# Performance work log

Hardware: AMD Instinct MI355X
Metric: run time of the kernel (lower is better)

The kernel has to match this reference:

```python
import jax, jax.numpy as jnp
import numpy as np

N, D, S, H, NH, HD, K = 1, 17, 128, 2048, 16, 128, 16
Dp = D - 1          # chunks with history (q[:, 1:])
Sk = 128            # kv chunk length
EPS = 1e-6


def setup_inputs() -> dict:
    key = jax.random.key(0)
    k0, k1, k2, k3, k4, k5 = jax.random.split(key, 6)
    return {
        "hidden_states": jax.random.normal(k0, (N, D, S, H), jnp.float32),
        "chunk_k": jax.random.normal(k1, (N * Dp * K, Sk, NH, HD), jnp.float32),
        "chunk_v": jax.random.normal(k2, (N * Dp * K, Sk, NH, HD), jnp.float32),
        "weights": jax.random.uniform(k3, (N, Dp, K), jnp.float32),
        "rms_weight": jnp.ones((H,), jnp.float32),
        "Wq": jax.random.normal(k4, (H, H), jnp.float32) * 0.02,
        "Wo": jax.random.normal(k5, (H, H), jnp.float32) * 0.02,
    }


def reference(hidden_states, chunk_k, chunk_v, weights, rms_weight, Wq, Wo):
    # RMSNorm (pre_norm)
    var = jnp.mean(hidden_states * hidden_states, axis=-1, keepdims=True)
    xn = hidden_states * jax.lax.rsqrt(var + EPS) * rms_weight
    # q projection: Linear stores (out, in) -> x @ W.T
    q = jnp.einsum('ndsh,eh->ndse', xn, Wq).reshape(N, D, S, NH, HD)
    # chunk_size (= D) > 1: drop the first chunk (no history)
    qd = q[:, 1:]                                      # (N, Dp, S, NH, HD)
    k = chunk_k.reshape(N, Dp, K, Sk, NH, HD)
    v = chunk_v.reshape(N, Dp, K, Sk, NH, HD)
    scale = 1.0 / np.sqrt(HD)
    # non-causal flash attention per (N, Dp, K) chunk
    scores = jnp.einsum('ndshe,ndkthe->ndkhst', qd, k) * scale
    p = jax.nn.softmax(scores, axis=-1)
    vals = jnp.einsum('ndkhst,ndkthe->ndkhse', p, v)   # (N, Dp, K, NH, S, HD)
    # weighted reduction over K history chunks
    wv = jnp.einsum('ndkhse,ndk->ndhse', vals, weights)
    o = wv.transpose(0, 1, 3, 2, 4).reshape(N, Dp * S, H)  # N (D S) (h d)
    o = jnp.einsum('nsh,eh->nse', o, Wo)
    # pad: first chunk (S = enc_chunk_size + 1 positions) gets zeros
    ret = jnp.zeros((N, D * S, H), o.dtype)
    ret = ret.at[:, -Dp * S:, :].set(o)
    return ret
```

## Files before the change

### kernel.cpp

```cpp
#include <hip/hip_runtime.h>
#include <hip/hip_bf16.h>
#include <math.h>


typedef __attribute__((ext_vector_type(8))) short bf16x8;
typedef __attribute__((ext_vector_type(4))) short bf16x4;
typedef __attribute__((ext_vector_type(4))) float f32x4;

__device__ __forceinline__ unsigned short f2bf(float f) {
    union { float f; unsigned u; } c; c.f = f;
    unsigned u = c.u + 0x7FFF + ((c.u >> 16) & 1);
    return (unsigned short)(u >> 16);
}

__global__ __launch_bounds__(256) void rms_kernel(const float* __restrict__ hs,
                                                  const float* __restrict__ rw,
                                                  unsigned short* __restrict__ xn) {
    int row = blockIdx.x;
    const float* x = hs + (size_t)(row + 128) * 2048;
    int tid = threadIdx.x;
    float4 a = ((const float4*)x)[tid * 2];
    float4 b = ((const float4*)x)[tid * 2 + 1];
    float ss = a.x*a.x + a.y*a.y + a.z*a.z + a.w*a.w
             + b.x*b.x + b.y*b.y + b.z*b.z + b.w*b.w;
#pragma unroll
    for (int m = 1; m < 64; m <<= 1) ss += __shfl_xor(ss, m);
    __shared__ float part[4];
    if ((tid & 63) == 0) part[tid >> 6] = ss;
    __syncthreads();
    float tot = part[0] + part[1] + part[2] + part[3];
    float rstd = rsqrtf(tot * (1.0f / 2048.0f) + 1e-6f);
    float4 wa = ((const float4*)rw)[tid * 2];
    float4 wb = ((const float4*)rw)[tid * 2 + 1];
    bf16x8 o;
    o[0] = (short)f2bf(a.x * rstd * wa.x);
    o[1] = (short)f2bf(a.y * rstd * wa.y);
    o[2] = (short)f2bf(a.z * rstd * wa.z);
    o[3] = (short)f2bf(a.w * rstd * wa.w);
    o[4] = (short)f2bf(b.x * rstd * wb.x);
    o[5] = (short)f2bf(b.y * rstd * wb.y);
    o[6] = (short)f2bf(b.z * rstd * wb.z);
    o[7] = (short)f2bf(b.w * rstd * wb.w);
    *reinterpret_cast<bf16x8*>(&xn[(size_t)row * 2048 + tid * 8]) = o;
}

__global__ __launch_bounds__(256) void cast_kernel(const float* __restrict__ in,
                                                   unsigned short* __restrict__ out) {
    size_t i = ((size_t)blockIdx.x * 256 + threadIdx.x) * 8;
    float4 a = *reinterpret_cast<const float4*>(in + i);
    float4 b = *reinterpret_cast<const float4*>(in + i + 4);
    bf16x8 o;
    o[0] = (short)f2bf(a.x); o[1] = (short)f2bf(a.y);
    o[2] = (short)f2bf(a.z); o[3] = (short)f2bf(a.w);
    o[4] = (short)f2bf(b.x); o[5] = (short)f2bf(b.y);
    o[6] = (short)f2bf(b.z); o[7] = (short)f2bf(b.w);
    *reinterpret_cast<bf16x8*>(out + i) = o;
}

template<int OUT_BF16>
__global__ __launch_bounds__(256) void gemm_bt(const unsigned short* __restrict__ A,
                                               const unsigned short* __restrict__ B,
                                               unsigned short* __restrict__ Cb,
                                               float* __restrict__ Cf) {
    __shared__ short As[128 * 72];
    __shared__ short Bs[128 * 72];
    int bm = (blockIdx.x >> 4) * 128;
    int bn = (blockIdx.x & 15) * 128;
    int tid = threadIdx.x;
    int lane = tid & 63, wid = tid >> 6;
    int wm = (wid >> 1) * 64, wn = (wid & 1) * 64;
    int r16 = lane & 15, g = lane >> 4;
    f32x4 acc[4][4] = {};

    for (int kt = 0; kt < 2048; kt += 64) {
#pragma unroll
        for (int p = 0; p < 4; ++p) {
            int idx = tid + p * 256;
            int r = idx >> 3, c = (idx & 7) * 8;
            *reinterpret_cast<bf16x8*>(&As[r * 72 + c]) =
                *reinterpret_cast<const bf16x8*>(&A[(size_t)(bm + r) * 2048 + kt + c]);
            *reinterpret_cast<bf16x8*>(&Bs[r * 72 + c]) =
                *reinterpret_cast<const bf16x8*>(&B[(size_t)(bn + r) * 2048 + kt + c]);
        }
        __syncthreads();
#pragma unroll
        for (int ks = 0; ks < 2; ++ks) {
            bf16x8 af[4], bfr[4];
#pragma unroll
            for (int i = 0; i < 4; ++i) {
                af[i]  = *reinterpret_cast<const bf16x8*>(&As[(wm + i * 16 + r16) * 72 + ks * 32 + g * 8]);
                bfr[i] = *reinterpret_cast<const bf16x8*>(&Bs[(wn + i * 16 + r16) * 72 + ks * 32 + g * 8]);
            }
#pragma unroll
            for (int i = 0; i < 4; ++i)
#pragma unroll
                for (int j = 0; j < 4; ++j)
                    acc[i][j] = __builtin_amdgcn_mfma_f32_16x16x32_bf16(af[i], bfr[j], acc[i][j], 0, 0, 0);
        }
        __syncthreads();
    }
#pragma unroll
    for (int i = 0; i < 4; ++i) {
        int row0 = bm + wm + i * 16 + g * 4;
#pragma unroll
        for (int j = 0; j < 4; ++j) {
            int col = bn + wn + j * 16 + r16;
#pragma unroll
            for (int rr = 0; rr < 4; ++rr) {
                float v = acc[i][j][rr];
                if (OUT_BF16) Cb[(size_t)(row0 + rr) * 2048 + col] = f2bf(v);
                else          Cf[(size_t)(row0 + rr) * 2048 + col] = v;
            }
        }
    }
}

__global__ __launch_bounds__(512) void attn_kernel(const unsigned short* __restrict__ q2d,
                                                   const float* __restrict__ ck,
                                                   const float* __restrict__ cv,
                                                   const float* __restrict__ wts,
                                                   unsigned short* __restrict__ o2d) {
    int dp = blockIdx.x >> 4;
    int h  = blockIdx.x & 15;
    int tid = threadIdx.x;
    int lane = tid & 63, w = tid >> 6;
    int r16 = lane & 15, g = lane >> 4;

    __shared__ short kbuf[128 * 136];
    __shared__ short vtbuf[128 * 136];
    __shared__ short pbuf[128 * 136];

    bf16x8 qf[4];
    {
        const unsigned short* qrow = q2d + (size_t)(dp * 128 + w * 16 + r16) * 2048 + h * 128 + g * 8;
#pragma unroll
        for (int ks = 0; ks < 4; ++ks)
            qf[ks] = *reinterpret_cast<const bf16x8*>(qrow + ks * 32);
    }
    f32x4 oacc[8] = {};
    const float sc = 0.088388347648318447f * 1.44269504088896f;

    for (int k = 0; k < 16; ++k) {
        size_t cbase = (size_t)(dp * 16 + k) * 128 * 2048 + h * 128;
#pragma unroll
        for (int p = 0; p < 8; ++p) {
            int t = p * 16 + (tid >> 5);
            int hd0 = (tid & 31) * 4;
            float4 v = *reinterpret_cast<const float4*>(&ck[cbase + (size_t)t * 2048 + hd0]);
            bf16x4 s4;
            s4[0] = (short)f2bf(v.x); s4[1] = (short)f2bf(v.y);
            s4[2] = (short)f2bf(v.z); s4[3] = (short)f2bf(v.w);
            *reinterpret_cast<bf16x4*>(&kbuf[t * 136 + hd0]) = s4;
        }
        {
            int hd = tid & 127;
            int tg = tid >> 7;
#pragma unroll
            for (int p = 0; p < 4; ++p) {
                int t0 = p * 32 + tg * 8;
                bf16x8 s8;
#pragma unroll
                for (int j = 0; j < 8; ++j)
                    s8[j] = (short)f2bf(cv[cbase + (size_t)(t0 + j) * 2048 + hd]);
                *reinterpret_cast<bf16x8*>(&vtbuf[hd * 136 + t0]) = s8;
            }
        }
        __syncthreads();

        f32x4 sacc[8] = {};
#pragma unroll
        for (int ks = 0; ks < 4; ++ks) {
#pragma unroll
            for (int nb = 0; nb < 8; ++nb) {
                bf16x8 kf = *reinterpret_cast<const bf16x8*>(&kbuf[(nb * 16 + r16) * 136 + ks * 32 + g * 8]);
                sacc[nb] = __builtin_amdgcn_mfma_f32_16x16x32_bf16(qf[ks], kf, sacc[nb], 0, 0, 0);
            }
        }

        float wdk = wts[dp * 16 + k];
        float fac[4];
#pragma unroll
        for (int r = 0; r < 4; ++r) {
            float m = sacc[0][r];
#pragma unroll
            for (int nb = 1; nb < 8; ++nb) m = fmaxf(m, sacc[nb][r]);
            m = fmaxf(m, __shfl_xor(m, 1));
            m = fmaxf(m, __shfl_xor(m, 2));
            m = fmaxf(m, __shfl_xor(m, 4));
            m = fmaxf(m, __shfl_xor(m, 8));
            float s = 0.f;
#pragma unroll
            for (int nb = 0; nb < 8; ++nb) {
                float p = exp2f((sacc[nb][r] - m) * sc);
                sacc[nb][r] = p;
                s += p;
            }
            s += __shfl_xor(s, 1);
            s += __shfl_xor(s, 2);
            s += __shfl_xor(s, 4);
            s += __shfl_xor(s, 8);
            fac[r] = wdk / s;
        }
#pragma unroll
        for (int r = 0; r < 4; ++r)
#pragma unroll
            for (int nb = 0; nb < 8; ++nb)
                pbuf[(w * 16 + g * 4 + r) * 136 + nb * 16 + r16] = (short)f2bf(sacc[nb][r] * fac[r]);

#pragma unroll
        for (int ks = 0; ks < 4; ++ks) {
            bf16x8 pf = *reinterpret_cast<const bf16x8*>(&pbuf[(w * 16 + r16) * 136 + ks * 32 + g * 8]);
#pragma unroll
            for (int nb = 0; nb < 8; ++nb) {
                bf16x8 vf = *reinterpret_cast<const bf16x8*>(&vtbuf[(nb * 16 + r16) * 136 + ks * 32 + g * 8]);
                oacc[nb] = __builtin_amdgcn_mfma_f32_16x16x32_bf16(pf, vf, oacc[nb], 0, 0, 0);
            }
        }
        __syncthreads();
    }

#pragma unroll
    for (int nb = 0; nb < 8; ++nb) {
#pragma unroll
        for (int rr = 0; rr < 4; ++rr) {
            int row = dp * 128 + w * 16 + g * 4 + rr;
            int col = h * 128 + nb * 16 + r16;
            o2d[(size_t)row * 2048 + col] = f2bf(oacc[nb][rr]);
        }
    }
}

extern "C" void kernel_launch(void* const* d_in, const int* in_sizes, int n_in,
                              void* d_out, int out_size, void* d_ws, size_t ws_size,
                              hipStream_t stream) {
    const float* hs  = (const float*)d_in[0];
    const float* ck  = (const float*)d_in[1];
    const float* cv  = (const float*)d_in[2];
    const float* wts = (const float*)d_in[3];
    const float* rw  = (const float*)d_in[4];
    const float* Wq  = (const float*)d_in[5];
    const float* Wo  = (const float*)d_in[6];
    float* out = (float*)d_out;

    char* ws = (char*)d_ws;
    unsigned short* xn  = (unsigned short*)(ws);
    unsigned short* wqb = (unsigned short*)(ws + (8u  << 20));
    unsigned short* qb  = (unsigned short*)(ws + (16u << 20));
    unsigned short* o2d = xn;
    unsigned short* wob = wqb;

    hipMemsetAsync(out, 0, (size_t)128 * 2048 * 4, stream);

    cast_kernel<<<2048, 256, 0, stream>>>(Wq, wqb);
    rms_kernel<<<2048, 256, 0, stream>>>(hs, rw, xn);
    gemm_bt<1><<<256, 256, 0, stream>>>(xn, wqb, qb, nullptr);
    attn_kernel<<<256, 512, 0, stream>>>(qb, ck, cv, wts, o2d);
    cast_kernel<<<2048, 256, 0, stream>>>(Wo, wob);
    gemm_bt<0><<<256, 256, 0, stream>>>(o2d, wob, nullptr, out + (size_t)128 * 2048);
}
```

Before: 659.2 us.

## Split-K GEMMs with atomic accumulation, LDS direct loads, and K/V register prefetch

Both projection GEMMs become a split-K kernel that launches 512 blocks instead of 256, each covering half of K and accumulating into zero-initialised fp32 output with atomicAdd. Tiles are loaded with global_load_lds straight into unpadded LDS. The q projection now lands in fp32 and is cast to bf16 inside attention. The attention kernel prefetches the next chunk's K/V into registers while computing the current one. The aim is better CU occupancy and overlap of loads with compute, at the cost of atomics, extra memsets, unpadded LDS bank conflicts and higher register pressure.

```diff
diff --git a/kernel.cpp b/kernel.cpp
--- a/kernel.cpp
+++ b/kernel.cpp
@@ -11,6 +11,11 @@
     union { float f; unsigned u; } c; c.f = f;
     unsigned u = c.u + 0x7FFF + ((c.u >> 16) & 1);
     return (unsigned short)(u >> 16);
+}
+
+__device__ __forceinline__ void gload16(const void* g, void* l) {
+    __builtin_amdgcn_global_load_lds((const __attribute__((address_space(1))) void*)g,
+                                     (__attribute__((address_space(3))) void*)l, 16, 0, 0);
 }
 
 __global__ __launch_bounds__(256) void rms_kernel(const float* __restrict__ hs,
@@ -57,30 +62,29 @@
     *reinterpret_cast<bf16x8*>(out + i) = o;
 }
 
-template<int OUT_BF16>
-__global__ __launch_bounds__(256) void gemm_bt(const unsigned short* __restrict__ A,
-                                               const unsigned short* __restrict__ B,
-                                               unsigned short* __restrict__ Cb,
-                                               float* __restrict__ Cf) {
-    __shared__ short As[128 * 72];
-    __shared__ short Bs[128 * 72];
-    int bm = (blockIdx.x >> 4) * 128;
-    int bn = (blockIdx.x & 15) * 128;
+__global__ __launch_bounds__(256, 2) void gemm_ks(const unsigned short* __restrict__ A,
+                                                  const unsigned short* __restrict__ B,
+                                                  float* __restrict__ C) {
+    __shared__ short As[128 * 64];
+    __shared__ short Bs[128 * 64];
+    int bid = blockIdx.x;
+    int ksl = bid & 1;
+    int bn = ((bid >> 1) & 15) * 128;
+    int bm = (bid >> 5) * 128;
     int tid = threadIdx.x;
     int lane = tid & 63, wid = tid >> 6;
     int wm = (wid >> 1) * 64, wn = (wid & 1) * 64;
     int r16 = lane & 15, g = lane >> 4;
     f32x4 acc[4][4] = {};
-
-    for (int kt = 0; kt < 2048; kt += 64) {
+    int k0 = ksl * 1024;
+
+    for (int kt = k0; kt < k0 + 1024; kt += 64) {
 #pragma unroll
         for (int p = 0; p < 4; ++p) {
-            int idx = tid + p * 256;
+            int idx = p * 256 + tid;
             int r = idx >> 3, c = (idx & 7) * 8;
-            *reinterpret_cast<bf16x8*>(&As[r * 72 + c]) =
-                *reinterpret_cast<const bf16x8*>(&A[(size_t)(bm + r) * 2048 + kt + c]);
-            *reinterpret_cast<bf16x8*>(&Bs[r * 72 + c]) =
-                *reinterpret_cast<const bf16x8*>(&B[(size_t)(bn + r) * 2048 + kt + c]);
+            gload16(&A[(size_t)(bm + r) * 2048 + kt + c], (void*)&As[idx * 8]);
+            gload16(&B[(size_t)(bn + r) * 2048 + kt + c], (void*)&Bs[idx * 8]);
         }
         __syncthreads();
 #pragma unroll
@@ -88,8 +92,8 @@
             bf16x8 af[4], bfr[4];
 #pragma unroll
             for (int i = 0; i < 4; ++i) {
-                af[i]  = *reinterpret_cast<const bf16x8*>(&As[(wm + i * 16 + r16) * 72 + ks * 32 + g * 8]);
-                bfr[i] = *reinterpret_cast<const bf16x8*>(&Bs[(wn + i * 16 + r16) * 72 + ks * 32 + g * 8]);
+                af[i]  = *reinterpret_cast<const bf16x8*>(&As[(wm + i * 16 + r16) * 64 + ks * 32 + g * 8]);
+                bfr[i] = *reinterpret_cast<const bf16x8*>(&Bs[(wn + i * 16 + r16) * 64 + ks * 32 + g * 8]);
             }
 #pragma unroll
             for (int i = 0; i < 4; ++i)
@@ -106,20 +110,17 @@
         for (int j = 0; j < 4; ++j) {
             int col = bn + wn + j * 16 + r16;
 #pragma unroll
-            for (int rr = 0; rr < 4; ++rr) {
-                float v = acc[i][j][rr];
-                if (OUT_BF16) Cb[(size_t)(row0 + rr) * 2048 + col] = f2bf(v);
-                else          Cf[(size_t)(row0 + rr) * 2048 + col] = v;
-            }
-        }
-    }
-}
-
-__global__ __launch_bounds__(512) void attn_kernel(const unsigned short* __restrict__ q2d,
-                                                   const float* __restrict__ ck,
-                                                   const float* __restrict__ cv,
-                                                   const float* __restrict__ wts,
-                                                   unsigned short* __restrict__ o2d) {
+            for (int rr = 0; rr < 4; ++rr)
+                atomicAdd(&C[(size_t)(row0 + rr) * 2048 + col], acc[i][j][rr]);
+        }
+    }
+}
+
+__global__ __launch_bounds__(512, 2) void attn_kernel(const float* __restrict__ qf,
+                                                      const float* __restrict__ ck,
+                                                      const float* __restrict__ cv,
+                                                      const float* __restrict__ wts,
+                                                      unsigned short* __restrict__ o2d) {
     int dp = blockIdx.x >> 4;
     int h  = blockIdx.x & 15;
     int tid = threadIdx.x;
@@ -130,42 +131,74 @@
     __shared__ short vtbuf[128 * 136];
     __shared__ short pbuf[128 * 136];
 
-    bf16x8 qf[4];
+    bf16x8 qfr[4];
     {
-        const unsigned short* qrow = q2d + (size_t)(dp * 128 + w * 16 + r16) * 2048 + h * 128 + g * 8;
-#pragma unroll
-        for (int ks = 0; ks < 4; ++ks)
-            qf[ks] = *reinterpret_cast<const bf16x8*>(qrow + ks * 32);
-    }
+        const float* qrow = qf + (size_t)(dp * 128 + w * 16 + r16) * 2048 + h * 128 + g * 8;
+#pragma unroll
+        for (int ks = 0; ks < 4; ++ks) {
+            float4 a = *reinterpret_cast<const float4*>(qrow + ks * 32);
+            float4 b = *reinterpret_cast<const float4*>(qrow + ks * 32 + 4);
+            bf16x8 q8;
+            q8[0] = (short)f2bf(a.x); q8[1] = (short)f2bf(a.y);
+            q8[2] = (short)f2bf(a.z); q8[3] = (short)f2bf(a.w);
+            q8[4] = (short)f2bf(b.x); q8[5] = (short)f2bf(b.y);
+            q8[6] = (short)f2bf(b.z); q8[7] = (short)f2bf(b.w);
+            qfr[ks] = q8;
+        }
+    }
+
+    int kt_row = tid >> 5;
+    int khd0   = (tid & 31) * 4;
+    int vhd    = tid & 127;
+    int vtg    = tid >> 7;
+
+    float4 kpre[8];
+    float  vpre[32];
+    {
+        size_t cb = (size_t)(dp * 16) * 128 * 2048 + h * 128;
+#pragma unroll
+        for (int p = 0; p < 8; ++p)
+            kpre[p] = *reinterpret_cast<const float4*>(&ck[cb + (size_t)(p * 16 + kt_row) * 2048 + khd0]);
+#pragma unroll
+        for (int p = 0; p < 4; ++p)
+#pragma unroll
+            for (int j = 0; j < 8; ++j)
+                vpre[p * 8 + j] = cv[cb + (size_t)(p * 32 + vtg * 8 + j) * 2048 + vhd];
+    }
+
     f32x4 oacc[8] = {};
     const float sc = 0.088388347648318447f * 1.44269504088896f;
 
     for (int k = 0; k < 16; ++k) {
-        size_t cbase = (size_t)(dp * 16 + k) * 128 * 2048 + h * 128;
 #pragma unroll
         for (int p = 0; p < 8; ++p) {
-            int t = p * 16 + (tid >> 5);
-            int hd0 = (tid & 31) * 4;
-            float4 v = *reinterpret_cast<const float4*>(&ck[cbase + (size_t)t * 2048 + hd0]);
+            int t = p * 16 + kt_row;
             bf16x4 s4;
-            s4[0] = (short)f2bf(v.x); s4[1] = (short)f2bf(v.y);
-            s4[2] = (short)f2bf(v.z); s4[3] = (short)f2bf(v.w);
-            *reinterpret_cast<bf16x4*>(&kbuf[t * 136 + hd0]) = s4;
-        }
-        {
-            int hd = tid & 127;
-            int tg = tid >> 7;
-#pragma unroll
-            for (int p = 0; p < 4; ++p) {
-                int t0 = p * 32 + tg * 8;
-                bf16x8 s8;
+            s4[0] = (short)f2bf(kpre[p].x); s4[1] = (short)f2bf(kpre[p].y);
+            s4[2] = (short)f2bf(kpre[p].z); s4[3] = (short)f2bf(kpre[p].w);
+            *reinterpret_cast<bf16x4*>(&kbuf[t * 136 + khd0]) = s4;
+        }
+#pragma unroll
+        for (int p = 0; p < 4; ++p) {
+            bf16x8 s8;
+#pragma unroll
+            for (int j = 0; j < 8; ++j)
+                s8[j] = (short)f2bf(vpre[p * 8 + j]);
+            *reinterpret_cast<bf16x8*>(&vtbuf[vhd * 136 + p * 32 + vtg * 8]) = s8;
+        }
+        __syncthreads();
+
+        if (k < 15) {
+            size_t cb = (size_t)(dp * 16 + k + 1) * 128 * 2048 + h * 128;
+#pragma unroll
+            for (int p = 0; p < 8; ++p)
+                kpre[p] = *reinterpret_cast<const float4*>(&ck[cb + (size_t)(p * 16 + kt_row) * 2048 + khd0]);
+#pragma unroll
+            for (int p = 0; p < 4; ++p)
 #pragma unroll
                 for (int j = 0; j < 8; ++j)
-                    s8[j] = (short)f2bf(cv[cbase + (size_t)(t0 + j) * 2048 + hd]);
-                *reinterpret_cast<bf16x8*>(&vtbuf[hd * 136 + t0]) = s8;
-            }
-        }
-        __syncthreads();
+                    vpre[p * 8 + j] = cv[cb + (size_t)(p * 32 + vtg * 8 + j) * 2048 + vhd];
+        }
 
         f32x4 sacc[8] = {};
 #pragma unroll
@@ -173,7 +206,7 @@
 #pragma unroll
             for (int nb = 0; nb < 8; ++nb) {
                 bf16x8 kf = *reinterpret_cast<const bf16x8*>(&kbuf[(nb * 16 + r16) * 136 + ks * 32 + g * 8]);
-                sacc[nb] = __builtin_amdgcn_mfma_f32_16x16x32_bf16(qf[ks], kf, sacc[nb], 0, 0, 0);
+                sacc[nb] = __builtin_amdgcn_mfma_f32_16x16x32_bf16(qfr[ks], kf, sacc[nb], 0, 0, 0);
             }
         }
 
@@ -245,16 +278,17 @@
     char* ws = (char*)d_ws;
     unsigned short* xn  = (unsigned short*)(ws);
     unsigned short* wqb = (unsigned short*)(ws + (8u  << 20));
-    unsigned short* qb  = (unsigned short*)(ws + (16u << 20));
+    float*          qf  = (float*)        (ws + (16u << 20));
     unsigned short* o2d = xn;
     unsigned short* wob = wqb;
 
-    hipMemsetAsync(out, 0, (size_t)128 * 2048 * 4, stream);
+    hipMemsetAsync(out, 0, (size_t)17 * 128 * 2048 * 4, stream);
+    hipMemsetAsync(qf, 0, (size_t)2048 * 2048 * 4, stream);
 
     cast_kernel<<<2048, 256, 0, stream>>>(Wq, wqb);
     rms_kernel<<<2048, 256, 0, stream>>>(hs, rw, xn);
-    gemm_bt<1><<<256, 256, 0, stream>>>(xn, wqb, qb, nullptr);
-    attn_kernel<<<256, 512, 0, stream>>>(qb, ck, cv, wts, o2d);
+    gemm_ks<<<512, 256, 0, stream>>>(xn, wqb, qf);
+    attn_kernel<<<256, 512, 0, stream>>>(qf, ck, cv, wts, o2d);
     cast_kernel<<<2048, 256, 0, stream>>>(Wo, wob);
-    gemm_bt<0><<<256, 256, 0, stream>>>(o2d, wob, nullptr, out + (size_t)128 * 2048);
-}
+    gemm_ks<<<512, 256, 0, stream>>>(o2d, wob, out + (size_t)128 * 2048);
+}
```

Result: no change. 662.4 us (+0.5%).
